# Optimization experiments

Measured on AMD Instinct MI355X. Metric: run time of the kernel, lower is better.

The kernel has to match this reference:

```python
import jax, jax.numpy as jnp
import numpy as np

B, T, C, H = 4, 2048, 512, 8
D = C // H  # head dim = 64

def setup_inputs() -> dict:
    key = jax.random.key(0)
    ks = jax.random.split(key, 6)
    x = jax.random.normal(ks[0], (B, T, C), dtype=jnp.float32)
    # per-batch graph adjacency mask: True = attend, False = masked
    adj_matrix = jax.random.bernoulli(ks[1], 0.5, (B, T, T))
    # ensure self-edges so no row is fully masked
    adj_matrix = adj_matrix | jnp.eye(T, dtype=bool)[None]
    s = 0.02
    w_qkv = jax.random.normal(ks[2], (C, 3 * C), dtype=jnp.float32) * s
    b_qkv = jnp.zeros((3 * C,), dtype=jnp.float32)
    w_proj = jax.random.normal(ks[3], (C, C), dtype=jnp.float32) * s
    b_proj = jnp.zeros((C,), dtype=jnp.float32)
    return {"x": x, "adj_matrix": adj_matrix, "w_qkv": w_qkv, "b_qkv": b_qkv,
            "w_proj": w_proj, "b_proj": b_proj}

def reference(x, adj_matrix, w_qkv, b_qkv, w_proj, b_proj):
    Bx, Tx, Cx = x.shape
    qkv = x @ w_qkv + b_qkv                       # [B,T,3C]
    q, k, v = jnp.split(qkv, 3, axis=-1)
    def heads(t):
        return t.reshape(Bx, Tx, H, D).transpose(0, 2, 1, 3)  # [B,H,T,D]
    q, k, v = heads(q), heads(k), heads(v)
    scale = 1.0 / jnp.sqrt(jnp.asarray(D, dtype=x.dtype))
    scores = jnp.einsum('bhtd,bhsd->bhts', q, k) * scale      # [B,H,T,T]
    neg = jnp.finfo(scores.dtype).min
    scores = jnp.where(adj_matrix[:, None, :, :], scores, neg)
    attn = jax.nn.softmax(scores, axis=-1)
    y = jnp.einsum('bhts,bhsd->bhtd', attn, v)                # [B,H,T,D]
    y = y.transpose(0, 2, 1, 3).reshape(Bx, Tx, Cx)           # [B,T,C]
    return y @ w_proj + b_proj
```

## Files before the change

### kernel.cpp

```cpp
#include <hip/hip_runtime.h>
#include <stdint.h>

typedef __attribute__((ext_vector_type(8))) __bf16 bf16x8;
typedef __attribute__((ext_vector_type(4))) __bf16 bf16x4;
typedef __attribute__((ext_vector_type(2))) __bf16 bf16x2;
typedef __attribute__((ext_vector_type(4))) float f32x4;
typedef __attribute__((ext_vector_type(16))) float f32x16;
typedef __attribute__((ext_vector_type(4))) unsigned u32x4;
typedef __attribute__((ext_vector_type(2))) int i32x2;

__device__ __forceinline__ unsigned short f2bf(float f) {
  unsigned u = __float_as_uint(f);
  u += 0x7FFFu + ((u >> 16) & 1u);
  return (unsigned short)(u >> 16);
}

__device__ __forceinline__ float exp2fast(float x) {
#if __has_builtin(__builtin_amdgcn_exp2f)
  return __builtin_amdgcn_exp2f(x);
#else
  return __expf(x * 0.6931471805599453f);
#endif
}

__device__ __forceinline__ void pl32swap(unsigned &a, unsigned &b) {
#if __has_builtin(__builtin_amdgcn_permlane32_swap)
  i32x2 r = __builtin_amdgcn_permlane32_swap((int)a, (int)b, false, false);
  a = (unsigned)r[0]; b = (unsigned)r[1];
#else
  asm volatile("v_permlane32_swap_b32 %0, %1" : "+v"(a), "+v"(b));
#endif
}

__device__ __forceinline__ int swz8(int r) { return (r & 7) ^ ((r >> 3) & 3); }

__device__ __forceinline__ void gload16(const unsigned short* src, unsigned short* ldsdst) {
  __builtin_amdgcn_global_load_lds(
      (const __attribute__((address_space(1))) unsigned int*)src,
      (__attribute__((address_space(3))) unsigned int*)ldsdst, 16, 0, 0);
}

__device__ __forceinline__ void stage8(const unsigned short* gbase, long long strideElems,
                                       unsigned short* ldsTile, int rowBase) {
  const int lane = threadIdx.x & 63;
  const int r = rowBase + (lane >> 3);
  const int oct = (lane & 7) ^ swz8(r);
  gload16(gbase + (long long)r * strideElems + oct * 8, ldsTile + rowBase * 64);
}


__global__ __launch_bounds__(256) void prep(const float* __restrict__ x,
                                            unsigned short* __restrict__ xb,
                                            const float* __restrict__ wq,
                                            unsigned short* __restrict__ wqt,
                                            const float* __restrict__ wp,
                                            unsigned short* __restrict__ wpt,
                                            const int* __restrict__ adj,
                                            unsigned long long* __restrict__ mb) {
  int blk = blockIdx.x;
  if (blk < 16384) {
    int tid = blk * 256 + threadIdx.x;
    int4 v = ((const int4*)adj)[tid];
    unsigned n = (v.x != 0 ? 1u : 0u) | (v.y != 0 ? 2u : 0u) |
                 (v.z != 0 ? 4u : 0u) | (v.w != 0 ? 8u : 0u);
    unsigned long long part = (unsigned long long)n << ((threadIdx.x & 15) * 4);
    part |= __shfl_xor(part, 1);
    part |= __shfl_xor(part, 2);
    part |= __shfl_xor(part, 4);
    part |= __shfl_xor(part, 8);
    if ((threadIdx.x & 15) == 0) mb[tid >> 4] = part;
    return;
  }
  blk -= 16384;
  if (blk < 4096) {
    int i = (blk * 256 + threadIdx.x) * 4;
    float4 v = *(const float4*)(x + i);
    ushort4 o;
    o.x = f2bf(v.x); o.y = f2bf(v.y); o.z = f2bf(v.z); o.w = f2bf(v.w);
    *(ushort4*)(xb + i) = o;
    return;
  }
  blk -= 4096;
  const float* w; unsigned short* wt; int N; int bx, by;
  if (blk < 768) { w = wq; wt = wqt; N = 1536; bx = blk & 15; by = blk >> 4; }
  else { blk -= 768; w = wp; wt = wpt; N = 512; bx = blk & 15; by = blk >> 4; }
  __shared__ float tile[32][33];
  int k0 = bx * 32, n0 = by * 32;
  int tx = threadIdx.x & 31, ty = threadIdx.x >> 5;
#pragma unroll
  for (int i = 0; i < 4; i++)
    tile[ty + i * 8][tx] = w[(long long)(k0 + ty + i * 8) * N + n0 + tx];
  __syncthreads();
#pragma unroll
  for (int i = 0; i < 4; i++)
    wt[(long long)(n0 + ty + i * 8) * 512 + k0 + tx] = f2bf(tile[tx][ty + i * 8]);
}


__device__ __forceinline__ void gemm_core(const unsigned short* __restrict__ A,
                                          const unsigned short* __restrict__ Wt,
                                          unsigned short* Al, unsigned short* Bl,
                                          int m0, int n0, f32x4 acc[4][4]) {
  const int lane = threadIdx.x & 63;
  const int wid = threadIdx.x >> 6;
  const int c = lane & 15, g = lane >> 4;
  const int wm = wid >> 1, wn = wid & 1;
  const unsigned short* Ab = A + (long long)m0 * 512;
  const unsigned short* Bb = Wt + (long long)n0 * 512;

  for (int k0 = 0; k0 < 512; k0 += 64) {
    __syncthreads();
#pragma unroll
    for (int i = 0; i < 4; i++) stage8(Ab + k0, 512, Al, wid * 32 + i * 8);
#pragma unroll
    for (int i = 0; i < 4; i++) stage8(Bb + k0, 512, Bl, wid * 32 + i * 8);
    asm volatile("s_waitcnt vmcnt(0)" ::: "memory");
    __syncthreads();
#pragma unroll
    for (int kk = 0; kk < 2; kk++) {
      bf16x8 af[4], bfr[4];
#pragma unroll
      for (int mi = 0; mi < 4; mi++) {
        int row = wm * 64 + mi * 16 + c;
        af[mi] = *(const bf16x8*)&Al[row * 64 + (((kk << 2) | g) ^ swz8(row)) * 8];
      }
#pragma unroll
      for (int ni = 0; ni < 4; ni++) {
        int row = wn * 64 + ni * 16 + c;
        bfr[ni] = *(const bf16x8*)&Bl[row * 64 + (((kk << 2) | g) ^ swz8(row)) * 8];
      }
#pragma unroll
      for (int mi = 0; mi < 4; mi++)
#pragma unroll
        for (int ni = 0; ni < 4; ni++)
          acc[mi][ni] = __builtin_amdgcn_mfma_f32_16x16x32_bf16(af[mi], bfr[ni], acc[mi][ni], 0, 0, 0);
    }
  }
}

__global__ __launch_bounds__(256) void gemm_qkv(const unsigned short* __restrict__ xb,
                                                const unsigned short* __restrict__ wqt,
                                                const float* __restrict__ bqkv,
                                                unsigned short* __restrict__ qb,
                                                unsigned short* __restrict__ kb,
                                                unsigned short* __restrict__ vtb) {
  __shared__ __align__(16) unsigned short Al[128 * 64];
  __shared__ __align__(16) unsigned short Bl[128 * 64];
  f32x4 acc[4][4] = {};
  int m0 = blockIdx.x * 128, n0 = blockIdx.y * 128;
  gemm_core(xb, wqt, Al, Bl, m0, n0, acc);
  const int lane = threadIdx.x & 63;
  const int wid = threadIdx.x >> 6;
  const int c = lane & 15, g = lane >> 4;
  const int wm = wid >> 1, wn = wid & 1;
#pragma unroll
  for (int ni = 0; ni < 4; ni++) {
    int n = n0 + wn * 64 + ni * 16 + c;
    float bv = bqkv[n];
    int which = n >> 9;
    int h = (n & 511) >> 6, d = n & 63;
#pragma unroll
    for (int mi = 0; mi < 4; mi++) {
      int mbase = m0 + wm * 64 + mi * 16 + g * 4;
      int b = mbase >> 11, t0 = mbase & 2047;
      int bh = b * 8 + h;
      if (which == 2) {
        ushort4 o;
        o.x = f2bf(acc[mi][ni][0] + bv); o.y = f2bf(acc[mi][ni][1] + bv);
        o.z = f2bf(acc[mi][ni][2] + bv); o.w = f2bf(acc[mi][ni][3] + bv);
        *(ushort4*)&vtb[((long long)bh * 64 + d) * 2048 + t0] = o;
      } else if (which == 0) {
#pragma unroll
        for (int j = 0; j < 4; j++)
          qb[(bh * 2048 + t0 + j) * 64 + d] = f2bf((acc[mi][ni][j] + bv) * 0.18033688011112042f);
      } else {
#pragma unroll
        for (int j = 0; j < 4; j++)
          kb[(bh * 2048 + t0 + j) * 64 + d] = f2bf(acc[mi][ni][j] + bv);
      }
    }
  }
}

__global__ __launch_bounds__(256) void gemm_proj(const unsigned short* __restrict__ yb,
                                                 const unsigned short* __restrict__ wpt,
                                                 const float* __restrict__ bproj,
                                                 float* __restrict__ out) {
  __shared__ __align__(16) unsigned short Al[128 * 64];
  __shared__ __align__(16) unsigned short Bl[128 * 64];
  f32x4 acc[4][4] = {};
  int m0 = blockIdx.x * 128, n0 = blockIdx.y * 128;
  gemm_core(yb, wpt, Al, Bl, m0, n0, acc);
  const int lane = threadIdx.x & 63;
  const int wid = threadIdx.x >> 6;
  const int c = lane & 15, g = lane >> 4;
  const int wm = wid >> 1, wn = wid & 1;
#pragma unroll
  for (int ni = 0; ni < 4; ni++) {
    int n = n0 + wn * 64 + ni * 16 + c;
    float bv = bproj[n];
#pragma unroll
    for (int mi = 0; mi < 4; mi++) {
      int mbase = m0 + wm * 64 + mi * 16 + g * 4;
#pragma unroll
      for (int j = 0; j < 4; j++)
        out[(long long)(mbase + j) * 512 + n] = acc[mi][ni][j] + bv;
    }
  }
}

__global__ __launch_bounds__(256, 4) void attn(const unsigned short* __restrict__ qb,
                                               const unsigned short* __restrict__ kb,
                                               const unsigned short* __restrict__ vtb,
                                               const unsigned long long* __restrict__ mbits,
                                               unsigned short* __restrict__ yb) {
  __shared__ __align__(16) unsigned short Kl[2][64 * 64];
  __shared__ __align__(16) unsigned short Vl[2][64 * 64];
  __shared__ __align__(16) float lut4[16][4];
  __shared__ float xl[2][128];
  const int lane = threadIdx.x & 63;
  const int w = threadIdx.x >> 6;
  const int half = w >> 1;
  const int wq = w & 1;
  const int l31 = lane & 31, h5 = lane >> 5;
  const int sA = swz8(l31);
  const int bid = blockIdx.x;
  const int bh = bid & 31;
  const int q0 = (bid >> 5) * 64;
  const int b = bh >> 3, h = bh & 7;
  const int qglob = q0 + wq * 32 + l31;

  if (threadIdx.x < 16) {
    int n = threadIdx.x;
#pragma unroll
    for (int j = 0; j < 4; j++) lut4[n][j] = ((n >> j) & 1) ? 0.0f : -1e30f;
  }

  const unsigned short* qptr = qb + ((long long)bh * 2048 + qglob) * 64;
  bf16x8 qf[4];
#pragma unroll
  for (int cc = 0; cc < 4; cc++) qf[cc] = *(const bf16x8*)(qptr + cc * 16 + h5 * 8);

  const unsigned long long* mrow =
      mbits + ((long long)b * 2048 + qglob) * 32 + half * 16;

  const int ln8 = lane >> 3, o8 = lane & 7;
  const unsigned short* kp0;
  const unsigned short* kp1;
  const unsigned short* kp2;
  const unsigned short* kp3;
  const unsigned short* vp0;
  const unsigned short* vp1;
  const unsigned short* vp2;
  const unsigned short* vp3;
  {
    const long long kb0 = (long long)bh * 2048 * 64 + (long long)(half * 1024) * 64;
    const long long vb0 = (long long)bh * 64 * 2048 + half * 1024;
    const int rr = wq * 32 + ln8;
    kp0 = kb + kb0 + (rr + 0) * 64 + ((o8 ^ ln8 ^ 0)) * 8;
    kp1 = kb + kb0 + (rr + 8) * 64 + ((o8 ^ ln8 ^ 1)) * 8;
    kp2 = kb + kb0 + (rr + 16) * 64 + ((o8 ^ ln8 ^ 2)) * 8;
    kp3 = kb + kb0 + (rr + 24) * 64 + ((o8 ^ ln8 ^ 3)) * 8;
    vp0 = vtb + vb0 + (long long)(rr + 0) * 2048 + ((o8 ^ ln8 ^ 0)) * 8;
    vp1 = vtb + vb0 + (long long)(rr + 8) * 2048 + ((o8 ^ ln8 ^ 1)) * 8;
    vp2 = vtb + vb0 + (long long)(rr + 16) * 2048 + ((o8 ^ ln8 ^ 2)) * 8;
    vp3 = vtb + vb0 + (long long)(rr + 24) * 2048 + ((o8 ^ ln8 ^ 3)) * 8;
  }
  unsigned short* Kd = &Kl[half][0] + wq * 32 * 64;
  unsigned short* Vd = &Vl[half][0] + wq * 32 * 64;

  const unsigned short* Kb = &Kl[half][0];
  const unsigned short* Vb = &Vl[half][0];

  const int uo0 = ((0 + h5) ^ sA) * 8, uo1 = ((2 + h5) ^ sA) * 8;
  const int uo2 = ((4 + h5) ^ sA) * 8, uo3 = ((6 + h5) ^ sA) * 8;

  f32x16 accO0 = {0,0,0,0, 0,0,0,0, 0,0,0,0, 0,0,0,0};
  f32x16 accO1 = {0,0,0,0, 0,0,0,0, 0,0,0,0, 0,0,0,0};
  float lsum = 0.0f;

  for (int t = 0; t < 16; ++t) {
    __syncthreads();
    gload16(kp0, Kd);        gload16(kp1, Kd + 8 * 64);
    gload16(kp2, Kd + 16 * 64); gload16(kp3, Kd + 24 * 64);
    gload16(vp0, Vd);        gload16(vp1, Vd + 8 * 64);
    gload16(vp2, Vd + 16 * 64); gload16(vp3, Vd + 24 * 64);
    kp0 += 4096; kp1 += 4096; kp2 += 4096; kp3 += 4096;
    vp0 += 64; vp1 += 64; vp2 += 64; vp3 += 64;
    unsigned long long mw = mrow[t];
    asm volatile("s_waitcnt vmcnt(0)" ::: "memory");
    __syncthreads();

    unsigned lo = (unsigned)mw, hi = (unsigned)(mw >> 32);
    unsigned pd[2][8];
    {
      f32x16 st;
#pragma unroll
      for (int j = 0; j < 4; j++) {
        f32x4 s = *(const f32x4*)lut4[(lo >> (8 * j + 4 * h5)) & 0xF];
#pragma unroll
        for (int i = 0; i < 4; i++) st[4 * j + i] = s[i];
      }
      __builtin_amdgcn_s_setprio(1);
#pragma unroll
      for (int cc = 0; cc < 4; cc++) {
        const int u = (cc == 0) ? uo0 : (cc == 1) ? uo1 : (cc == 2) ? uo2 : uo3;
        bf16x8 kf = *(const bf16x8*)&Kb[l31 * 64 + u];
        st = __builtin_amdgcn_mfma_f32_32x32x16_bf16(kf, qf[cc], st, 0, 0, 0);
      }
      __builtin_amdgcn_s_setprio(0);
#pragma unroll
      for (int m = 0; m < 8; m++) {
        float p0 = exp2fast(st[2 * m]);
        float p1 = exp2fast(st[2 * m + 1]);
        lsum += (p0 + p1);
        bf16x2 v0 = {(__bf16)p0, (__bf16)p1};
        pd[0][m] = __builtin_bit_cast(unsigned, v0);
      }
    }
    {
      f32x16 st;
#pragma unroll
      for (int j = 0; j < 4; j++) {
        f32x4 s = *(const f32x4*)lut4[(hi >> (8 * j + 4 * h5)) & 0xF];
#pragma unroll
        for (int i = 0; i < 4; i++) st[4 * j + i] = s[i];
      }
      __builtin_amdgcn_s_setprio(1);
#pragma unroll
      for (int cc = 0; cc < 4; cc++) {
        const int u = (cc == 0) ? uo0 : (cc == 1) ? uo1 : (cc == 2) ? uo2 : uo3;
        bf16x8 kf = *(const bf16x8*)&Kb[(32 + l31) * 64 + u];
        st = __builtin_amdgcn_mfma_f32_32x32x16_bf16(kf, qf[cc], st, 0, 0, 0);
      }
      __builtin_amdgcn_s_setprio(0);
#pragma unroll
      for (int m = 0; m < 8; m++) {
        float p0 = exp2fast(st[2 * m]);
        float p1 = exp2fast(st[2 * m + 1]);
        lsum += (p0 + p1);
        bf16x2 v0 = {(__bf16)p0, (__bf16)p1};
        pd[1][m] = __builtin_bit_cast(unsigned, v0);
      }
    }
#pragma unroll
    for (int ot = 0; ot < 2; ot++)
#pragma unroll
      for (int hc = 0; hc < 2; hc++) {
        pl32swap(pd[ot][4 * hc + 0], pd[ot][4 * hc + 2]);
        pl32swap(pd[ot][4 * hc + 1], pd[ot][4 * hc + 3]);
      }
    __builtin_amdgcn_s_setprio(1);
#pragma unroll
    for (int cc = 0; cc < 4; cc++) {
      u32x4 pu = {pd[cc >> 1][4 * (cc & 1) + 0], pd[cc >> 1][4 * (cc & 1) + 1],
                  pd[cc >> 1][4 * (cc & 1) + 2], pd[cc >> 1][4 * (cc & 1) + 3]};
      bf16x8 pf = __builtin_bit_cast(bf16x8, pu);
      const int u = (cc == 0) ? uo0 : (cc == 1) ? uo1 : (cc == 2) ? uo2 : uo3;
      bf16x8 vf0 = *(const bf16x8*)&Vb[l31 * 64 + u];
      bf16x8 vf1 = *(const bf16x8*)&Vb[(32 + l31) * 64 + u];
      accO0 = __builtin_amdgcn_mfma_f32_32x32x16_bf16(vf0, pf, accO0, 0, 0, 0);
      accO1 = __builtin_amdgcn_mfma_f32_32x32x16_bf16(vf1, pf, accO1, 0, 0, 0);
    }
    __builtin_amdgcn_s_setprio(0);
  }

  float lh = lsum + __shfl_xor(lsum, 32);

  __syncthreads();
  float* xch = (float*)&Kl[0][0];
  {
    float* dst = xch + (w * 64 + lane) * 16;
    f32x16 give = half ? accO0 : accO1;
#pragma unroll
    for (int m = 0; m < 4; m++)
      *(f32x4*)(dst + 4 * m) = f32x4{give[4 * m + 0], give[4 * m + 1],
                                     give[4 * m + 2], give[4 * m + 3]};
    xl[half][wq * 64 + lane] = lh;
  }
  __syncthreads();
  {
    const float* src = xch + (((half ^ 1) * 2 + wq) * 64 + lane) * 16;
    float linv = 1.0f / (lh + xl[half ^ 1][wq * 64 + lane]);
    f32x16 keep = half ? accO1 : accO0;
    unsigned short* yrow = yb + ((long long)(b * 2048 + qglob)) * 512 + h * 64 + half * 32;
#pragma unroll
    for (int m = 0; m < 4; m++) {
      f32x4 a = *(const f32x4*)(src + 4 * m);
      int d0 = 8 * m + 4 * h5;
      bf16x4 o = {(__bf16)((keep[4 * m + 0] + a[0]) * linv),
                  (__bf16)((keep[4 * m + 1] + a[1]) * linv),
                  (__bf16)((keep[4 * m + 2] + a[2]) * linv),
                  (__bf16)((keep[4 * m + 3] + a[3]) * linv)};
      *(bf16x4*)&yrow[d0] = o;
    }
  }
}


extern "C" void kernel_launch(void* const* d_in, const int* in_sizes, int n_in,
                              void* d_out, int out_size, void* d_ws, size_t ws_size,
                              hipStream_t stream) {
  const float* x      = (const float*)d_in[0];
  const int*   adj    = (const int*)d_in[1];
  const float* w_qkv  = (const float*)d_in[2];
  const float* b_qkv  = (const float*)d_in[3];
  const float* w_proj = (const float*)d_in[4];
  const float* b_proj = (const float*)d_in[5];
  float* out = (float*)d_out;

  char* ws = (char*)d_ws;
  unsigned short* xb  = (unsigned short*)(ws);
  unsigned short* qb  = (unsigned short*)(ws + 8388608);
  unsigned short* kbf = (unsigned short*)(ws + 16777216);
  unsigned short* vtb = (unsigned short*)(ws + 25165824);
  unsigned short* wqt = (unsigned short*)(ws + 33554432);
  unsigned short* wpt = (unsigned short*)(ws + 35127296);
  unsigned long long* mb = (unsigned long long*)(ws + 35651584);
  unsigned short* yb = xb;

  prep<<<dim3(21504), dim3(256), 0, stream>>>(x, xb, w_qkv, wqt, w_proj, wpt, adj, mb);
  gemm_qkv<<<dim3(64, 12), dim3(256), 0, stream>>>(xb, wqt, b_qkv, qb, kbf, vtb);
  attn<<<dim3(1024), dim3(256), 0, stream>>>(qb, kbf, vtb, mb, yb);
  gemm_proj<<<dim3(64, 4), dim3(256), 0, stream>>>(yb, wpt, b_proj, out);
}
```

Before: 115.2 us.

## Prefetch next K/V tile into registers during compute, then write LDS

Replaces the synchronous global-to-LDS tile load with a register-staged prefetch. The next tile's K and V are loaded into registers at the top of each iteration, overlapping the QK and PV MFMA work, and written to LDS after a barrier at the end. This hides global memory latency that was previously exposed by the vmcnt(0) wait. It costs extra VGPRs, so launch bounds drop from 4 to 3 blocks per SM, lowering occupancy.

```diff
diff --git a/kernel.cpp b/kernel.cpp
--- a/kernel.cpp
+++ b/kernel.cpp
@@ -209,7 +209,7 @@
   }
 }
 
-__global__ __launch_bounds__(256, 4) void attn(const unsigned short* __restrict__ qb,
+__global__ __launch_bounds__(256, 3) void attn(const unsigned short* __restrict__ qb,
                                                const unsigned short* __restrict__ kb,
                                                const unsigned short* __restrict__ vtb,
                                                const unsigned long long* __restrict__ mbits,
@@ -245,29 +245,17 @@
       mbits + ((long long)b * 2048 + qglob) * 32 + half * 16;
 
   const int ln8 = lane >> 3, o8 = lane & 7;
-  const unsigned short* kp0;
-  const unsigned short* kp1;
-  const unsigned short* kp2;
-  const unsigned short* kp3;
-  const unsigned short* vp0;
-  const unsigned short* vp1;
-  const unsigned short* vp2;
-  const unsigned short* vp3;
-  {
-    const long long kb0 = (long long)bh * 2048 * 64 + (long long)(half * 1024) * 64;
-    const long long vb0 = (long long)bh * 64 * 2048 + half * 1024;
-    const int rr = wq * 32 + ln8;
-    kp0 = kb + kb0 + (rr + 0) * 64 + ((o8 ^ ln8 ^ 0)) * 8;
-    kp1 = kb + kb0 + (rr + 8) * 64 + ((o8 ^ ln8 ^ 1)) * 8;
-    kp2 = kb + kb0 + (rr + 16) * 64 + ((o8 ^ ln8 ^ 2)) * 8;
-    kp3 = kb + kb0 + (rr + 24) * 64 + ((o8 ^ ln8 ^ 3)) * 8;
-    vp0 = vtb + vb0 + (long long)(rr + 0) * 2048 + ((o8 ^ ln8 ^ 0)) * 8;
-    vp1 = vtb + vb0 + (long long)(rr + 8) * 2048 + ((o8 ^ ln8 ^ 1)) * 8;
-    vp2 = vtb + vb0 + (long long)(rr + 16) * 2048 + ((o8 ^ ln8 ^ 2)) * 8;
-    vp3 = vtb + vb0 + (long long)(rr + 24) * 2048 + ((o8 ^ ln8 ^ 3)) * 8;
-  }
-  unsigned short* Kd = &Kl[half][0] + wq * 32 * 64;
-  unsigned short* Vd = &Vl[half][0] + wq * 32 * 64;
+  const unsigned short* kp[4];
+  const unsigned short* vp[4];
+#pragma unroll
+  for (int i = 0; i < 4; i++) {
+    int r = wq * 32 + i * 8 + ln8;
+    int c8 = o8 ^ ln8 ^ i;
+    kp[i] = kb + ((long long)bh * 2048 + half * 1024 + r) * 64 + c8 * 8;
+    vp[i] = vtb + ((long long)bh * 64 + r) * 2048 + half * 1024 + c8 * 8;
+  }
+  unsigned short* kw = &Kl[half][(wq * 32) * 64] + lane * 8;
+  unsigned short* vw = &Vl[half][(wq * 32) * 64] + lane * 8;
 
   const unsigned short* Kb = &Kl[half][0];
   const unsigned short* Vb = &Vl[half][0];
@@ -279,17 +267,35 @@
   f32x16 accO1 = {0,0,0,0, 0,0,0,0, 0,0,0,0, 0,0,0,0};
   float lsum = 0.0f;
 
+  u32x4 ldk0, ldk1, ldk2, ldk3, ldv0, ldv1, ldv2, ldv3;
+
+#define LOADREGS() do {                                   \
+    ldk0 = *(const u32x4*)kp[0]; ldk1 = *(const u32x4*)kp[1]; \
+    ldk2 = *(const u32x4*)kp[2]; ldk3 = *(const u32x4*)kp[3]; \
+    ldv0 = *(const u32x4*)vp[0]; ldv1 = *(const u32x4*)vp[1]; \
+    ldv2 = *(const u32x4*)vp[2]; ldv3 = *(const u32x4*)vp[3]; \
+    kp[0] += 4096; kp[1] += 4096; kp[2] += 4096; kp[3] += 4096; \
+    vp[0] += 64; vp[1] += 64; vp[2] += 64; vp[3] += 64; } while (0)
+
+#define WRITELDS() do {                                   \
+    *(u32x4*)(kw)            = ldk0;                      \
+    *(u32x4*)(kw + 512)      = ldk1;                      \
+    *(u32x4*)(kw + 1024)     = ldk2;                      \
+    *(u32x4*)(kw + 1536)     = ldk3;                      \
+    *(u32x4*)(vw)            = ldv0;                      \
+    *(u32x4*)(vw + 512)      = ldv1;                      \
+    *(u32x4*)(vw + 1024)     = ldv2;                      \
+    *(u32x4*)(vw + 1536)     = ldv3; } while (0)
+
+  LOADREGS();
+  WRITELDS();
+  asm volatile("s_waitcnt lgkmcnt(0)" ::: "memory");
+  __builtin_amdgcn_sched_barrier(0);
+  __builtin_amdgcn_s_barrier();
+
   for (int t = 0; t < 16; ++t) {
-    __syncthreads();
-    gload16(kp0, Kd);        gload16(kp1, Kd + 8 * 64);
-    gload16(kp2, Kd + 16 * 64); gload16(kp3, Kd + 24 * 64);
-    gload16(vp0, Vd);        gload16(vp1, Vd + 8 * 64);
-    gload16(vp2, Vd + 16 * 64); gload16(vp3, Vd + 24 * 64);
-    kp0 += 4096; kp1 += 4096; kp2 += 4096; kp3 += 4096;
-    vp0 += 64; vp1 += 64; vp2 += 64; vp3 += 64;
+    if (t < 15) LOADREGS();
     unsigned long long mw = mrow[t];
-    asm volatile("s_waitcnt vmcnt(0)" ::: "memory");
-    __syncthreads();
 
     unsigned lo = (unsigned)mw, hi = (unsigned)(mw >> 32);
     unsigned pd[2][8];
@@ -363,7 +369,19 @@
       accO1 = __builtin_amdgcn_mfma_f32_32x32x16_bf16(vf1, pf, accO1, 0, 0, 0);
     }
     __builtin_amdgcn_s_setprio(0);
-  }
+
+    asm volatile("s_waitcnt lgkmcnt(0)" ::: "memory");
+    __builtin_amdgcn_s_barrier();
+    if (t < 15) {
+      WRITELDS();
+      asm volatile("s_waitcnt lgkmcnt(0)" ::: "memory");
+      __builtin_amdgcn_sched_barrier(0);
+      __builtin_amdgcn_s_barrier();
+    }
+  }
+
+#undef LOADREGS
+#undef WRITELDS
 
   float lh = lsum + __shfl_xor(lsum, 32);
 
```

New measurement: 122.4 us. 6.2% more time.

## Store V in MFMA fragment order and double-buffer K tiles in attention

Applied to the files above, without the earlier changes.

The QKV GEMM now writes V directly in the per-lane MFMA operand layout, so the attention kernel loads V fragments straight from global memory into registers and no longer stages V in shared memory. The freed LDS is used to double-buffer K, so the next tile's K load is issued before the current tile is computed, with one barrier per tile instead of two. This is meant to hide global-load latency and cut LDS traffic and synchronisation. In exchange it adds register pressure from holding eight V fragments per tile, and the V global loads are now exposed without LDS staging.

```diff
diff --git a/kernel.cpp b/kernel.cpp
--- a/kernel.cpp
+++ b/kernel.cpp
@@ -143,7 +143,7 @@
                                                 const float* __restrict__ bqkv,
                                                 unsigned short* __restrict__ qb,
                                                 unsigned short* __restrict__ kb,
-                                                unsigned short* __restrict__ vtb) {
+                                                unsigned short* __restrict__ vfb) {
   __shared__ __align__(16) unsigned short Al[128 * 64];
   __shared__ __align__(16) unsigned short Bl[128 * 64];
   f32x4 acc[4][4] = {};
@@ -165,10 +165,14 @@
       int b = mbase >> 11, t0 = mbase & 2047;
       int bh = b * 8 + h;
       if (which == 2) {
+        int t = t0 >> 6, wv = t0 & 63, f = wv >> 3;
+        int cc = f >> 1, h5p = f & 1, s = d >> 5;
+        int ln = h5p * 32 + (d & 31), el = t0 & 7;
+        long long fi = (((long long)bh * 32 + t) * 2 + s) * 4 + cc;
         ushort4 o;
         o.x = f2bf(acc[mi][ni][0] + bv); o.y = f2bf(acc[mi][ni][1] + bv);
         o.z = f2bf(acc[mi][ni][2] + bv); o.w = f2bf(acc[mi][ni][3] + bv);
-        *(ushort4*)&vtb[((long long)bh * 64 + d) * 2048 + t0] = o;
+        *(ushort4*)&vfb[(fi * 64 + ln) * 8 + el] = o;
       } else if (which == 0) {
 #pragma unroll
         for (int j = 0; j < 4; j++)
@@ -211,11 +215,10 @@
 
 __global__ __launch_bounds__(256, 4) void attn(const unsigned short* __restrict__ qb,
                                                const unsigned short* __restrict__ kb,
-                                               const unsigned short* __restrict__ vtb,
+                                               const unsigned short* __restrict__ vfb,
                                                const unsigned long long* __restrict__ mbits,
                                                unsigned short* __restrict__ yb) {
-  __shared__ __align__(16) unsigned short Kl[2][64 * 64];
-  __shared__ __align__(16) unsigned short Vl[2][64 * 64];
+  __shared__ __align__(16) unsigned short Kl[2][2][64 * 64];
   __shared__ __align__(16) float lut4[16][4];
   __shared__ float xl[2][128];
   const int lane = threadIdx.x & 63;
@@ -249,28 +252,21 @@
   const unsigned short* kp1;
   const unsigned short* kp2;
   const unsigned short* kp3;
-  const unsigned short* vp0;
-  const unsigned short* vp1;
-  const unsigned short* vp2;
-  const unsigned short* vp3;
   {
     const long long kb0 = (long long)bh * 2048 * 64 + (long long)(half * 1024) * 64;
-    const long long vb0 = (long long)bh * 64 * 2048 + half * 1024;
     const int rr = wq * 32 + ln8;
     kp0 = kb + kb0 + (rr + 0) * 64 + ((o8 ^ ln8 ^ 0)) * 8;
     kp1 = kb + kb0 + (rr + 8) * 64 + ((o8 ^ ln8 ^ 1)) * 8;
     kp2 = kb + kb0 + (rr + 16) * 64 + ((o8 ^ ln8 ^ 2)) * 8;
     kp3 = kb + kb0 + (rr + 24) * 64 + ((o8 ^ ln8 ^ 3)) * 8;
-    vp0 = vtb + vb0 + (long long)(rr + 0) * 2048 + ((o8 ^ ln8 ^ 0)) * 8;
-    vp1 = vtb + vb0 + (long long)(rr + 8) * 2048 + ((o8 ^ ln8 ^ 1)) * 8;
-    vp2 = vtb + vb0 + (long long)(rr + 16) * 2048 + ((o8 ^ ln8 ^ 2)) * 8;
-    vp3 = vtb + vb0 + (long long)(rr + 24) * 2048 + ((o8 ^ ln8 ^ 3)) * 8;
-  }
-  unsigned short* Kd = &Kl[half][0] + wq * 32 * 64;
-  unsigned short* Vd = &Vl[half][0] + wq * 32 * 64;
-
-  const unsigned short* Kb = &Kl[half][0];
-  const unsigned short* Vb = &Vl[half][0];
+  }
+  const unsigned short* vfp =
+      vfb + ((long long)(bh * 32 + half * 16) * 8) * 512 + lane * 8;
+
+  unsigned short* Kd0 = &Kl[half][0][(wq * 32) * 64];
+  unsigned short* Kd1 = &Kl[half][1][(wq * 32) * 64];
+  const unsigned short* Kb0 = &Kl[half][0][0];
+  const unsigned short* Kb1 = &Kl[half][1][0];
 
   const int uo0 = ((0 + h5) ^ sA) * 8, uo1 = ((2 + h5) ^ sA) * 8;
   const int uo2 = ((4 + h5) ^ sA) * 8, uo3 = ((6 + h5) ^ sA) * 8;
@@ -279,96 +275,113 @@
   f32x16 accO1 = {0,0,0,0, 0,0,0,0, 0,0,0,0, 0,0,0,0};
   float lsum = 0.0f;
 
-  for (int t = 0; t < 16; ++t) {
-    __syncthreads();
-    gload16(kp0, Kd);        gload16(kp1, Kd + 8 * 64);
-    gload16(kp2, Kd + 16 * 64); gload16(kp3, Kd + 24 * 64);
-    gload16(vp0, Vd);        gload16(vp1, Vd + 8 * 64);
-    gload16(vp2, Vd + 16 * 64); gload16(vp3, Vd + 24 * 64);
-    kp0 += 4096; kp1 += 4096; kp2 += 4096; kp3 += 4096;
-    vp0 += 64; vp1 += 64; vp2 += 64; vp3 += 64;
-    unsigned long long mw = mrow[t];
-    asm volatile("s_waitcnt vmcnt(0)" ::: "memory");
-    __syncthreads();
-
-    unsigned lo = (unsigned)mw, hi = (unsigned)(mw >> 32);
-    unsigned pd[2][8];
-    {
-      f32x16 st;
-#pragma unroll
-      for (int j = 0; j < 4; j++) {
-        f32x4 s = *(const f32x4*)lut4[(lo >> (8 * j + 4 * h5)) & 0xF];
-#pragma unroll
-        for (int i = 0; i < 4; i++) st[4 * j + i] = s[i];
-      }
-      __builtin_amdgcn_s_setprio(1);
-#pragma unroll
-      for (int cc = 0; cc < 4; cc++) {
-        const int u = (cc == 0) ? uo0 : (cc == 1) ? uo1 : (cc == 2) ? uo2 : uo3;
-        bf16x8 kf = *(const bf16x8*)&Kb[l31 * 64 + u];
-        st = __builtin_amdgcn_mfma_f32_32x32x16_bf16(kf, qf[cc], st, 0, 0, 0);
-      }
-      __builtin_amdgcn_s_setprio(0);
-#pragma unroll
-      for (int m = 0; m < 8; m++) {
-        float p0 = exp2fast(st[2 * m]);
-        float p1 = exp2fast(st[2 * m + 1]);
-        lsum += (p0 + p1);
-        bf16x2 v0 = {(__bf16)p0, (__bf16)p1};
-        pd[0][m] = __builtin_bit_cast(unsigned, v0);
-      }
-    }
-    {
-      f32x16 st;
-#pragma unroll
-      for (int j = 0; j < 4; j++) {
-        f32x4 s = *(const f32x4*)lut4[(hi >> (8 * j + 4 * h5)) & 0xF];
-#pragma unroll
-        for (int i = 0; i < 4; i++) st[4 * j + i] = s[i];
-      }
-      __builtin_amdgcn_s_setprio(1);
-#pragma unroll
-      for (int cc = 0; cc < 4; cc++) {
-        const int u = (cc == 0) ? uo0 : (cc == 1) ? uo1 : (cc == 2) ? uo2 : uo3;
-        bf16x8 kf = *(const bf16x8*)&Kb[(32 + l31) * 64 + u];
-        st = __builtin_amdgcn_mfma_f32_32x32x16_bf16(kf, qf[cc], st, 0, 0, 0);
-      }
-      __builtin_amdgcn_s_setprio(0);
-#pragma unroll
-      for (int m = 0; m < 8; m++) {
-        float p0 = exp2fast(st[2 * m]);
-        float p1 = exp2fast(st[2 * m + 1]);
-        lsum += (p0 + p1);
-        bf16x2 v0 = {(__bf16)p0, (__bf16)p1};
-        pd[1][m] = __builtin_bit_cast(unsigned, v0);
-      }
-    }
-#pragma unroll
-    for (int ot = 0; ot < 2; ot++)
-#pragma unroll
-      for (int hc = 0; hc < 2; hc++) {
-        pl32swap(pd[ot][4 * hc + 0], pd[ot][4 * hc + 2]);
-        pl32swap(pd[ot][4 * hc + 1], pd[ot][4 * hc + 3]);
-      }
-    __builtin_amdgcn_s_setprio(1);
-#pragma unroll
-    for (int cc = 0; cc < 4; cc++) {
-      u32x4 pu = {pd[cc >> 1][4 * (cc & 1) + 0], pd[cc >> 1][4 * (cc & 1) + 1],
-                  pd[cc >> 1][4 * (cc & 1) + 2], pd[cc >> 1][4 * (cc & 1) + 3]};
-      bf16x8 pf = __builtin_bit_cast(bf16x8, pu);
-      const int u = (cc == 0) ? uo0 : (cc == 1) ? uo1 : (cc == 2) ? uo2 : uo3;
-      bf16x8 vf0 = *(const bf16x8*)&Vb[l31 * 64 + u];
-      bf16x8 vf1 = *(const bf16x8*)&Vb[(32 + l31) * 64 + u];
-      accO0 = __builtin_amdgcn_mfma_f32_32x32x16_bf16(vf0, pf, accO0, 0, 0, 0);
-      accO1 = __builtin_amdgcn_mfma_f32_32x32x16_bf16(vf1, pf, accO1, 0, 0, 0);
-    }
-    __builtin_amdgcn_s_setprio(0);
-  }
+#define STAGEK(KD) do {                          \
+    gload16(kp0, (KD));                          \
+    gload16(kp1, (KD) + 8 * 64);                 \
+    gload16(kp2, (KD) + 16 * 64);                \
+    gload16(kp3, (KD) + 24 * 64);                \
+    kp0 += 4096; kp1 += 4096; kp2 += 4096; kp3 += 4096; } while (0)
+
+#define TILE(KBC, KDN, MWC, MWN, T) do {                                  \
+    if ((T) < 15) STAGEK(KDN);                                            \
+    bf16x8 vf0[4], vf1[4];                                                \
+    _Pragma("unroll")                                                     \
+    for (int cc = 0; cc < 4; cc++) {                                      \
+      vf0[cc] = *(const bf16x8*)(vfp + cc * 512);                         \
+      vf1[cc] = *(const bf16x8*)(vfp + 2048 + cc * 512);                  \
+    }                                                                     \
+    vfp += 4096;                                                          \
+    if ((T) < 15) MWN = mrow[(T) + 1];                                    \
+    unsigned lo = (unsigned)MWC, hi = (unsigned)(MWC >> 32);              \
+    unsigned pd[2][8];                                                    \
+    {                                                                     \
+      f32x16 st;                                                          \
+      _Pragma("unroll")                                                   \
+      for (int j = 0; j < 4; j++) {                                       \
+        f32x4 s = *(const f32x4*)lut4[(lo >> (8 * j + 4 * h5)) & 0xF];    \
+        _Pragma("unroll")                                                 \
+        for (int i = 0; i < 4; i++) st[4 * j + i] = s[i];                 \
+      }                                                                   \
+      __builtin_amdgcn_s_setprio(1);                                      \
+      _Pragma("unroll")                                                   \
+      for (int cc = 0; cc < 4; cc++) {                                    \
+        const int u = (cc == 0) ? uo0 : (cc == 1) ? uo1 : (cc == 2) ? uo2 : uo3; \
+        bf16x8 kf = *(const bf16x8*)&(KBC)[l31 * 64 + u];                 \
+        st = __builtin_amdgcn_mfma_f32_32x32x16_bf16(kf, qf[cc], st, 0, 0, 0); \
+      }                                                                   \
+      __builtin_amdgcn_s_setprio(0);                                      \
+      _Pragma("unroll")                                                   \
+      for (int m = 0; m < 8; m++) {                                       \
+        float p0 = exp2fast(st[2 * m]);                                   \
+        float p1 = exp2fast(st[2 * m + 1]);                               \
+        lsum += (p0 + p1);                                                \
+        bf16x2 v0 = {(__bf16)p0, (__bf16)p1};                             \
+        pd[0][m] = __builtin_bit_cast(unsigned, v0);                      \
+      }                                                                   \
+    }                                                                     \
+    {                                                                     \
+      f32x16 st;                                                          \
+      _Pragma("unroll")                                                   \
+      for (int j = 0; j < 4; j++) {                                       \
+        f32x4 s = *(const f32x4*)lut4[(hi >> (8 * j + 4 * h5)) & 0xF];    \
+        _Pragma("unroll")                                                 \
+        for (int i = 0; i < 4; i++) st[4 * j + i] = s[i];                 \
+      }                                                                   \
+      __builtin_amdgcn_s_setprio(1);                                      \
+      _Pragma("unroll")                                                   \
+      for (int cc = 0; cc < 4; cc++) {                                    \
+        const int u = (cc == 0) ? uo0 : (cc == 1) ? uo1 : (cc == 2) ? uo2 : uo3; \
+        bf16x8 kf = *(const bf16x8*)&(KBC)[(32 + l31) * 64 + u];          \
+        st = __builtin_amdgcn_mfma_f32_32x32x16_bf16(kf, qf[cc], st, 0, 0, 0); \
+      }                                                                   \
+      __builtin_amdgcn_s_setprio(0);                                      \
+      _Pragma("unroll")                                                   \
+      for (int m = 0; m < 8; m++) {                                       \
+        float p0 = exp2fast(st[2 * m]);                                   \
+        float p1 = exp2fast(st[2 * m + 1]);                               \
+        lsum += (p0 + p1);                                                \
+        bf16x2 v0 = {(__bf16)p0, (__bf16)p1};                             \
+        pd[1][m] = __builtin_bit_cast(unsigned, v0);                      \
+      }                                                                   \
+    }                                                                     \
+    _Pragma("unroll")                                                     \
+    for (int ot = 0; ot < 2; ot++)                                        \
+      _Pragma("unroll")                                                   \
+      for (int hc = 0; hc < 2; hc++) {                                    \
+        pl32swap(pd[ot][4 * hc + 0], pd[ot][4 * hc + 2]);                 \
+        pl32swap(pd[ot][4 * hc + 1], pd[ot][4 * hc + 3]);                 \
+      }                                                                   \
+    __builtin_amdgcn_s_setprio(1);                                        \
+    _Pragma("unroll")                                                     \
+    for (int cc = 0; cc < 4; cc++) {                                      \
+      u32x4 pu = {pd[cc >> 1][4 * (cc & 1) + 0], pd[cc >> 1][4 * (cc & 1) + 1], \
+                  pd[cc >> 1][4 * (cc & 1) + 2], pd[cc >> 1][4 * (cc & 1) + 3]}; \
+      bf16x8 pf = __builtin_bit_cast(bf16x8, pu);                         \
+      accO0 = __builtin_amdgcn_mfma_f32_32x32x16_bf16(vf0[cc], pf, accO0, 0, 0, 0); \
+      accO1 = __builtin_amdgcn_mfma_f32_32x32x16_bf16(vf1[cc], pf, accO1, 0, 0, 0); \
+    }                                                                     \
+    __builtin_amdgcn_s_setprio(0);                                        \
+    asm volatile("s_waitcnt lgkmcnt(0)" ::: "memory");                    \
+    __builtin_amdgcn_s_barrier(); } while (0)
+
+  unsigned long long mwA, mwB;
+  STAGEK(Kd0);
+  mwA = mrow[0];
+  asm volatile("s_waitcnt vmcnt(0)" ::: "memory");
+  __builtin_amdgcn_s_barrier();
+
+  for (int k = 0; k < 8; ++k) {
+    TILE(Kb0, Kd1, mwA, mwB, 2 * k);
+    TILE(Kb1, Kd0, mwB, mwA, 2 * k + 1);
+  }
+
+#undef TILE
+#undef STAGEK
 
   float lh = lsum + __shfl_xor(lsum, 32);
 
   __syncthreads();
-  float* xch = (float*)&Kl[0][0];
+  float* xch = (float*)&Kl[0][0][0];
   {
     float* dst = xch + (w * 64 + lane) * 16;
     f32x16 give = half ? accO0 : accO1;
@@ -413,14 +426,14 @@
   unsigned short* xb  = (unsigned short*)(ws);
   unsigned short* qb  = (unsigned short*)(ws + 8388608);
   unsigned short* kbf = (unsigned short*)(ws + 16777216);
-  unsigned short* vtb = (unsigned short*)(ws + 25165824);
+  unsigned short* vfb = (unsigned short*)(ws + 25165824);
   unsigned short* wqt = (unsigned short*)(ws + 33554432);
   unsigned short* wpt = (unsigned short*)(ws + 35127296);
   unsigned long long* mb = (unsigned long long*)(ws + 35651584);
   unsigned short* yb = xb;
 
   prep<<<dim3(21504), dim3(256), 0, stream>>>(x, xb, w_qkv, wqt, w_proj, wpt, adj, mb);
-  gemm_qkv<<<dim3(64, 12), dim3(256), 0, stream>>>(xb, wqt, b_qkv, qb, kbf, vtb);
-  attn<<<dim3(1024), dim3(256), 0, stream>>>(qb, kbf, vtb, mb, yb);
+  gemm_qkv<<<dim3(64, 12), dim3(256), 0, stream>>>(xb, wqt, b_qkv, qb, kbf, vfb);
+  attn<<<dim3(1024), dim3(256), 0, stream>>>(qb, kbf, vfb, mb, yb);
   gemm_proj<<<dim3(64, 4), dim3(256), 0, stream>>>(yb, wpt, b_proj, out);
 }
```

After: 191.8 us. +66.4%, slower.
